# Kernel tuning notes

Hardware: AMD Instinct MI355X
Metric: run time of the kernel (lower is better)

Reference implementation:

```python
import jax, jax.numpy as jnp
import numpy as np

NEG_INF = -1e9
LEAKY_SLOPE = 0.2


def setup_inputs() -> dict:
    key = jax.random.key(0)
    k1, k2, k3, k4, k5 = jax.random.split(key, 5)
    B, N, F_in, F_out = 8, 2048, 256, 256
    x = jax.random.normal(k1, (B, N, F_in), dtype=jnp.float32)
    adj = jax.random.randint(k2, (B, N, N), 0, 2, dtype=jnp.int32)
    W = jax.random.normal(k3, (F_out, F_in), dtype=jnp.float32) * 0.05
    a_src = jax.random.normal(k4, (F_out,), dtype=jnp.float32) * 0.05
    a_dst = jax.random.normal(k5, (F_out,), dtype=jnp.float32) * 0.05
    return {"x": x, "adj": adj, "W": W, "a_src": a_src, "a_dst": a_dst}


def reference(x, adj, W, a_src, a_dst):
    # h: (B, N, F_out)
    h = jnp.einsum("bnf,of->bno", x, W)
    # a([h_i ; h_j]) == h_i @ a_src + h_j @ a_dst  (avoids O(N^2, 2F) concat)
    s_src = h @ a_src  # (B, N) score contribution of row node i
    s_dst = h @ a_dst  # (B, N) score contribution of col node j
    e = s_src[:, :, None] + s_dst[:, None, :]  # (B, N, N)
    e = jax.nn.leaky_relu(e, negative_slope=LEAKY_SLOPE)
    e = jnp.where(adj == 0, jnp.float32(NEG_INF), e)
    alpha = jax.nn.softmax(e, axis=-1)  # dropout is identity in eval mode
    h_prime = jnp.einsum("bij,bjo->bio", alpha, h)
    return h_prime
```

## Files before the change

kernel.cpp:

```cpp
#include <hip/hip_runtime.h>
#include <hip/hip_bf16.h>
#include <cstdint>
#include <cstddef>

typedef __attribute__((ext_vector_type(8))) short short8;
typedef __attribute__((ext_vector_type(4))) short short4v;
typedef __attribute__((ext_vector_type(4))) float floatx4;
typedef __attribute__((ext_vector_type(16))) float floatx16;
typedef unsigned short ushort_t;

#define LOG2E 1.44269504088896340736f

__device__ __forceinline__ unsigned short f2bf(float f) {
    unsigned u = __float_as_uint(f);
    u += 0x7FFFu + ((u >> 16) & 1u);
    return (unsigned short)(u >> 16);
}
__device__ __forceinline__ float bf2f(unsigned short s) {
    return __uint_as_float(((unsigned)s) << 16);
}

__global__ __launch_bounds__(1024) void gemm_h(const float* __restrict__ x,
                                               const float* __restrict__ W,
                                               ushort_t* __restrict__ hT,
                                               const float* __restrict__ a_src,
                                               const float* __restrict__ a_dst,
                                               float* __restrict__ s_src,
                                               float* __restrict__ s_dst) {
    const int tid = threadIdx.x;
    const int w = tid >> 6, lane = tid & 63;
    const int q = lane >> 4, t16 = lane & 15;
    const int jg = w >> 2, og = w & 3;

    __shared__ ushort_t wt[256][72];
    __shared__ float sred[2][4][64];

    const int jrow = blockIdx.x * 64 + jg * 16 + t16;
    const float* xr = x + (size_t)jrow * 256 + q * 8;
    short8 af[8];
#pragma unroll
    for (int kb = 0; kb < 8; ++kb) {
        float4 v0 = *(const float4*)(xr + kb * 32);
        float4 v1 = *(const float4*)(xr + kb * 32 + 4);
        short8 a;
        a[0] = (short)f2bf(v0.x); a[1] = (short)f2bf(v0.y);
        a[2] = (short)f2bf(v0.z); a[3] = (short)f2bf(v0.w);
        a[4] = (short)f2bf(v1.x); a[5] = (short)f2bf(v1.y);
        a[6] = (short)f2bf(v1.z); a[7] = (short)f2bf(v1.w);
        af[kb] = a;
    }

    floatx4 acc[4] = {};
#pragma unroll
    for (int kp = 0; kp < 4; ++kp) {
        if (kp) __syncthreads();
#pragma unroll
        for (int r = 0; r < 2; ++r) {
            int G = tid + 1024 * r;
            int row = G >> 3, g = G & 7;
            const float* wsrc = W + (size_t)row * 256 + kp * 64 + g * 8;
            float4 f0 = *(const float4*)(wsrc);
            float4 f1 = *(const float4*)(wsrc + 4);
            short8 wv;
            wv[0] = (short)f2bf(f0.x); wv[1] = (short)f2bf(f0.y);
            wv[2] = (short)f2bf(f0.z); wv[3] = (short)f2bf(f0.w);
            wv[4] = (short)f2bf(f1.x); wv[5] = (short)f2bf(f1.y);
            wv[6] = (short)f2bf(f1.z); wv[7] = (short)f2bf(f1.w);
            *(short8*)(&wt[row][g * 8]) = wv;
        }
        __syncthreads();
#pragma unroll
        for (int ks = 0; ks < 2; ++ks) {
#pragma unroll
            for (int ct = 0; ct < 4; ++ct) {
                short8 bf = *(const short8*)(&wt[og * 64 + ct * 16 + t16][ks * 32 + q * 8]);
                acc[ct] = __builtin_amdgcn_mfma_f32_16x16x32_bf16(af[kp * 2 + ks], bf, acc[ct], 0, 0, 0);
            }
        }
    }

    const int jbase = blockIdx.x * 64 + jg * 16 + q * 4;
    const int b = jbase >> 11, jj = jbase & 2047;
#pragma unroll
    for (int ct = 0; ct < 4; ++ct) {
        const int o = og * 64 + ct * 16 + t16;
        short4v sv;
        sv[0] = (short)f2bf(acc[ct][0]);
        sv[1] = (short)f2bf(acc[ct][1]);
        sv[2] = (short)f2bf(acc[ct][2]);
        sv[3] = (short)f2bf(acc[ct][3]);
        *(short4v*)(hT + ((size_t)b * 256 + o) * 2048 + jj) = sv;
    }

    float psv[4] = {}, pdv[4] = {};
#pragma unroll
    for (int ct = 0; ct < 4; ++ct) {
        const int o = og * 64 + ct * 16 + t16;
        float as = a_src[o], ad = a_dst[o];
#pragma unroll
        for (int r = 0; r < 4; ++r) {
            psv[r] = __fmaf_rn(acc[ct][r], as, psv[r]);
            pdv[r] = __fmaf_rn(acc[ct][r], ad, pdv[r]);
        }
    }
#pragma unroll
    for (int m = 1; m < 16; m <<= 1) {
#pragma unroll
        for (int r = 0; r < 4; ++r) {
            psv[r] += __shfl_xor(psv[r], m);
            pdv[r] += __shfl_xor(pdv[r], m);
        }
    }
    if (t16 == 0) {
#pragma unroll
        for (int r = 0; r < 4; ++r) {
            sred[0][og][jg * 16 + q * 4 + r] = psv[r];
            sred[1][og][jg * 16 + q * 4 + r] = pdv[r];
        }
    }
    __syncthreads();
    if (tid < 64) {
        float ss = sred[0][0][tid] + sred[0][1][tid] + sred[0][2][tid] + sred[0][3][tid];
        float dd = sred[1][0][tid] + sred[1][1][tid] + sred[1][2][tid] + sred[1][3][tid];
        s_src[blockIdx.x * 64 + tid] = ss;
        s_dst[blockIdx.x * 64 + tid] = dd;
    }
}

__global__ __launch_bounds__(1024) void attn(const ushort_t* __restrict__ hT,
                                             const int* __restrict__ adj,
                                             const float* __restrict__ s_src,
                                             const float* __restrict__ s_dst,
                                             float* __restrict__ out) {
    const int tid = threadIdx.x;
    const int w = tid >> 6;
    const int lane = tid & 63;
    const int l5 = lane & 31, hi = lane >> 5;
    const int b = blockIdx.x;
    const int i0 = blockIdx.y * 64;

    __shared__ ushort_t ps[2][64][72];
    __shared__ float sdl[2048];
    __shared__ float rls[64];

    const float* sdb = s_dst + (size_t)b * 2048;
    {
        int idx = tid * 2;
        float2 v = *(const float2*)(sdb + idx);
        v.x *= LOG2E; v.y *= LOG2E;
        *(float2*)(&sdl[idx]) = v;
    }

    const int ip = tid >> 4, jq = tid & 15;
    const float si = s_src[(size_t)b * 2048 + i0 + ip] * LOG2E;
    const int* adjr = adj + ((size_t)b * 2048 + i0 + ip) * 2048 + jq * 4;

    const int osub = (w & 7) * 32, ih = (w >> 3) * 32;
    const ushort_t* hTg = hT + ((size_t)b * 256 + osub + l5) * 2048 + hi * 8;

    floatx16 acc = {};
    float lsum = 0.f;
    int4 aE, aO;
    short8 af0[4], af1[4];

    aE = *(const int4*)(adjr);
    aO = *(const int4*)(adjr + 64);
#pragma unroll
    for (int ks = 0; ks < 4; ++ks)
        af0[ks] = *(const short8*)(hTg + ks * 16);
    __syncthreads();

#pragma unroll 1
    for (int it = 0; it < 16; ++it) {
        const int sc = it * 2;
        {
            float4 sd = *(const float4*)(&sdl[sc * 64 + jq * 4]);
            float sv[4] = {sd.x, sd.y, sd.z, sd.w};
            int mv[4] = {aE.x, aE.y, aE.z, aE.w};
            short4v pv;
#pragma unroll
            for (int e = 0; e < 4; ++e) {
                float t = si + sv[e];
                float lr = fmaxf(t, 0.2f * t);
                float pe = __builtin_amdgcn_exp2f(lr);
                pe = (mv[e] != 0) ? pe : 0.0f;
                unsigned short u = f2bf(pe);
                lsum += bf2f(u);
                pv[e] = (short)u;
            }
            *(short4v*)(&ps[0][ip][jq * 4]) = pv;
        }
        {
            const int nc = (sc + 2 < 32) ? sc + 2 : 31;
            aE = *(const int4*)(adjr + (size_t)nc * 64);
        }
#pragma unroll
        for (int ks = 0; ks < 4; ++ks)
            af1[ks] = *(const short8*)(hTg + (size_t)(sc + 1) * 64 + ks * 16);
        __syncthreads();
#pragma unroll
        for (int ks = 0; ks < 4; ++ks) {
            short8 bfr = *(const short8*)(&ps[0][ih + l5][ks * 16 + hi * 8]);
            acc = __builtin_amdgcn_mfma_f32_32x32x16_bf16(af0[ks], bfr, acc, 0, 0, 0);
        }
        {
            float4 sd = *(const float4*)(&sdl[(sc + 1) * 64 + jq * 4]);
            float sv[4] = {sd.x, sd.y, sd.z, sd.w};
            int mv[4] = {aO.x, aO.y, aO.z, aO.w};
            short4v pv;
#pragma unroll
            for (int e = 0; e < 4; ++e) {
                float t = si + sv[e];
                float lr = fmaxf(t, 0.2f * t);
                float pe = __builtin_amdgcn_exp2f(lr);
                pe = (mv[e] != 0) ? pe : 0.0f;
                unsigned short u = f2bf(pe);
                lsum += bf2f(u);
                pv[e] = (short)u;
            }
            *(short4v*)(&ps[1][ip][jq * 4]) = pv;
        }
        {
            const int nc = (sc + 3 < 32) ? sc + 3 : 31;
            aO = *(const int4*)(adjr + (size_t)nc * 64);
        }
        {
            const int na = (sc + 2 < 32) ? sc + 2 : 31;
#pragma unroll
            for (int ks = 0; ks < 4; ++ks)
                af0[ks] = *(const short8*)(hTg + (size_t)na * 64 + ks * 16);
        }
        __syncthreads();
#pragma unroll
        for (int ks = 0; ks < 4; ++ks) {
            short8 bfr = *(const short8*)(&ps[1][ih + l5][ks * 16 + hi * 8]);
            acc = __builtin_amdgcn_mfma_f32_32x32x16_bf16(af1[ks], bfr, acc, 0, 0, 0);
        }
    }

#pragma unroll
    for (int m = 1; m < 16; m <<= 1) lsum += __shfl_xor(lsum, m);
    if (jq == 0) rls[ip] = lsum;
    __syncthreads();

    {
        const int i = ih + l5;
        const float s = rls[i];
        const float rl = (s > 0.f) ? 1.0f / s : 0.0f;
        float* orow = out + ((size_t)b * 2048 + i0 + i) * 256 + osub;
#pragma unroll
        for (int rq = 0; rq < 4; ++rq) {
            floatx4 v;
            v[0] = acc[rq * 4 + 0] * rl;
            v[1] = acc[rq * 4 + 1] * rl;
            v[2] = acc[rq * 4 + 2] * rl;
            v[3] = acc[rq * 4 + 3] * rl;
            *(floatx4*)(orow + rq * 8 + hi * 4) = v;
        }
    }
}

extern "C" void kernel_launch(void* const* d_in, const int* in_sizes, int n_in,
                              void* d_out, int out_size, void* d_ws, size_t ws_size,
                              hipStream_t stream) {
    const float* x     = (const float*)d_in[0];
    const int*   adj   = (const int*)d_in[1];
    const float* W     = (const float*)d_in[2];
    const float* a_src = (const float*)d_in[3];
    const float* a_dst = (const float*)d_in[4];
    float* out = (float*)d_out;

    char* ws = (char*)d_ws;
    ushort_t* hT = (ushort_t*)ws;
    float* s_src = (float*)(ws + (size_t)8 * 1024 * 1024);
    float* s_dst = s_src + 16384;

    gemm_h<<<256, 1024, 0, stream>>>(x, W, hT, a_src, a_dst, s_src, s_dst);
    attn<<<dim3(8, 32), 1024, 0, stream>>>(hT, adj, s_src, s_dst, out);
}
```

Before: 273.2 us.

## Split attention into smaller blocks over rows and feature halves with LDS-staged h

The attention kernel now uses 256-thread blocks covering 32 query rows and half of the output features, launching four times as many blocks. The h tiles are staged through double-buffered shared memory instead of per-wave register loads, with a 32-column j chunk. This aims to raise occupancy and CU utilisation. In exchange, adjacency reads and exp computation are duplicated across the two feature halves.

```diff
diff --git a/kernel.cpp b/kernel.cpp
--- a/kernel.cpp
+++ b/kernel.cpp
@@ -127,54 +127,62 @@
     }
 }
 
-__global__ __launch_bounds__(1024) void attn(const ushort_t* __restrict__ hT,
-                                             const int* __restrict__ adj,
-                                             const float* __restrict__ s_src,
-                                             const float* __restrict__ s_dst,
-                                             float* __restrict__ out) {
+__global__ __launch_bounds__(256) void attn(const ushort_t* __restrict__ hT,
+                                            const int* __restrict__ adj,
+                                            const float* __restrict__ s_src,
+                                            const float* __restrict__ s_dst,
+                                            float* __restrict__ out) {
     const int tid = threadIdx.x;
     const int w = tid >> 6;
     const int lane = tid & 63;
     const int l5 = lane & 31, hi = lane >> 5;
     const int b = blockIdx.x;
-    const int i0 = blockIdx.y * 64;
-
-    __shared__ ushort_t ps[2][64][72];
+    const int i0 = blockIdx.y * 32;
+    const int ob = blockIdx.z * 128;
+
+    __shared__ ushort_t hts[2][128][40];
+    __shared__ ushort_t ps[2][32][40];
     __shared__ float sdl[2048];
-    __shared__ float rls[64];
+    __shared__ float rls[32];
 
     const float* sdb = s_dst + (size_t)b * 2048;
     {
-        int idx = tid * 2;
-        float2 v = *(const float2*)(sdb + idx);
-        v.x *= LOG2E; v.y *= LOG2E;
-        *(float2*)(&sdl[idx]) = v;
-    }
-
-    const int ip = tid >> 4, jq = tid & 15;
+        float4 v0 = *(const float4*)(sdb + tid * 8);
+        float4 v1 = *(const float4*)(sdb + tid * 8 + 4);
+        v0.x *= LOG2E; v0.y *= LOG2E; v0.z *= LOG2E; v0.w *= LOG2E;
+        v1.x *= LOG2E; v1.y *= LOG2E; v1.z *= LOG2E; v1.w *= LOG2E;
+        *(float4*)(&sdl[tid * 8]) = v0;
+        *(float4*)(&sdl[tid * 8 + 4]) = v1;
+    }
+
+    const int ip = tid >> 3, jq = tid & 7;
     const float si = s_src[(size_t)b * 2048 + i0 + ip] * LOG2E;
     const int* adjr = adj + ((size_t)b * 2048 + i0 + ip) * 2048 + jq * 4;
 
-    const int osub = (w & 7) * 32, ih = (w >> 3) * 32;
-    const ushort_t* hTg = hT + ((size_t)b * 256 + osub + l5) * 2048 + hi * 8;
+    const int srow = tid >> 2, sseg = tid & 3;
+    const ushort_t* hTg0 = hT + ((size_t)b * 256 + ob + srow) * 2048 + sseg * 8;
+    const ushort_t* hTg1 = hTg0 + (size_t)64 * 2048;
+
+    const int osub = w * 32;
 
     floatx16 acc = {};
     float lsum = 0.f;
     int4 aE, aO;
-    short8 af0[4], af1[4];
+    int4 hA0, hA1;
 
     aE = *(const int4*)(adjr);
-    aO = *(const int4*)(adjr + 64);
-#pragma unroll
-    for (int ks = 0; ks < 4; ++ks)
-        af0[ks] = *(const short8*)(hTg + ks * 16);
+    aO = *(const int4*)(adjr + 32);
+    hA0 = *(const int4*)(hTg0);
+    hA1 = *(const int4*)(hTg1);
     __syncthreads();
 
 #pragma unroll 1
-    for (int it = 0; it < 16; ++it) {
-        const int sc = it * 2;
+    for (int it = 0; it < 32; ++it) {
+        const int c = it * 2;
+        *(int4*)(&hts[0][srow][sseg * 8]) = hA0;
+        *(int4*)(&hts[0][srow + 64][sseg * 8]) = hA1;
         {
-            float4 sd = *(const float4*)(&sdl[sc * 64 + jq * 4]);
+            float4 sd = *(const float4*)(&sdl[c * 32 + jq * 4]);
             float sv[4] = {sd.x, sd.y, sd.z, sd.w};
             int mv[4] = {aE.x, aE.y, aE.z, aE.w};
             short4v pv;
@@ -190,21 +198,20 @@
             }
             *(short4v*)(&ps[0][ip][jq * 4]) = pv;
         }
+        hA0 = *(const int4*)(hTg0 + (size_t)(c + 1) * 32);
+        hA1 = *(const int4*)(hTg1 + (size_t)(c + 1) * 32);
+        aE = *(const int4*)(adjr + (size_t)((c + 2 < 64) ? c + 2 : 63) * 32);
+        __syncthreads();
+#pragma unroll
+        for (int ks = 0; ks < 2; ++ks) {
+            short8 afr = *(const short8*)(&hts[0][osub + l5][ks * 16 + hi * 8]);
+            short8 bfr = *(const short8*)(&ps[0][l5][ks * 16 + hi * 8]);
+            acc = __builtin_amdgcn_mfma_f32_32x32x16_bf16(afr, bfr, acc, 0, 0, 0);
+        }
+        *(int4*)(&hts[1][srow][sseg * 8]) = hA0;
+        *(int4*)(&hts[1][srow + 64][sseg * 8]) = hA1;
         {
-            const int nc = (sc + 2 < 32) ? sc + 2 : 31;
-            aE = *(const int4*)(adjr + (size_t)nc * 64);
-        }
-#pragma unroll
-        for (int ks = 0; ks < 4; ++ks)
-            af1[ks] = *(const short8*)(hTg + (size_t)(sc + 1) * 64 + ks * 16);
-        __syncthreads();
-#pragma unroll
-        for (int ks = 0; ks < 4; ++ks) {
-            short8 bfr = *(const short8*)(&ps[0][ih + l5][ks * 16 + hi * 8]);
-            acc = __builtin_amdgcn_mfma_f32_32x32x16_bf16(af0[ks], bfr, acc, 0, 0, 0);
-        }
-        {
-            float4 sd = *(const float4*)(&sdl[(sc + 1) * 64 + jq * 4]);
+            float4 sd = *(const float4*)(&sdl[(c + 1) * 32 + jq * 4]);
             float sv[4] = {sd.x, sd.y, sd.z, sd.w};
             int mv[4] = {aO.x, aO.y, aO.z, aO.w};
             short4v pv;
@@ -221,33 +228,30 @@
             *(short4v*)(&ps[1][ip][jq * 4]) = pv;
         }
         {
-            const int nc = (sc + 3 < 32) ? sc + 3 : 31;
-            aO = *(const int4*)(adjr + (size_t)nc * 64);
-        }
-        {
-            const int na = (sc + 2 < 32) ? sc + 2 : 31;
-#pragma unroll
-            for (int ks = 0; ks < 4; ++ks)
-                af0[ks] = *(const short8*)(hTg + (size_t)na * 64 + ks * 16);
-        }
+            const int nh = (c + 2 < 64) ? c + 2 : 63;
+            hA0 = *(const int4*)(hTg0 + (size_t)nh * 32);
+            hA1 = *(const int4*)(hTg1 + (size_t)nh * 32);
+        }
+        aO = *(const int4*)(adjr + (size_t)((c + 3 < 64) ? c + 3 : 63) * 32);
         __syncthreads();
 #pragma unroll
-        for (int ks = 0; ks < 4; ++ks) {
-            short8 bfr = *(const short8*)(&ps[1][ih + l5][ks * 16 + hi * 8]);
-            acc = __builtin_amdgcn_mfma_f32_32x32x16_bf16(af1[ks], bfr, acc, 0, 0, 0);
-        }
-    }
-
-#pragma unroll
-    for (int m = 1; m < 16; m <<= 1) lsum += __shfl_xor(lsum, m);
+        for (int ks = 0; ks < 2; ++ks) {
+            short8 afr = *(const short8*)(&hts[1][osub + l5][ks * 16 + hi * 8]);
+            short8 bfr = *(const short8*)(&ps[1][l5][ks * 16 + hi * 8]);
+            acc = __builtin_amdgcn_mfma_f32_32x32x16_bf16(afr, bfr, acc, 0, 0, 0);
+        }
+    }
+
+#pragma unroll
+    for (int m = 1; m < 8; m <<= 1) lsum += __shfl_xor(lsum, m);
     if (jq == 0) rls[ip] = lsum;
     __syncthreads();
 
     {
-        const int i = ih + l5;
+        const int i = l5;
         const float s = rls[i];
         const float rl = (s > 0.f) ? 1.0f / s : 0.0f;
-        float* orow = out + ((size_t)b * 2048 + i0 + i) * 256 + osub;
+        float* orow = out + ((size_t)b * 2048 + i0 + i) * 256 + ob + osub;
 #pragma unroll
         for (int rq = 0; rq < 4; ++rq) {
             floatx4 v;
@@ -276,5 +280,5 @@
     float* s_dst = s_src + 16384;
 
     gemm_h<<<256, 1024, 0, stream>>>(x, W, hT, a_src, a_dst, s_src, s_dst);
-    attn<<<dim3(8, 32), 1024, 0, stream>>>(hT, adj, s_src, s_dst, out);
-}
+    attn<<<dim3(8, 64, 2), 256, 0, stream>>>(hT, adj, s_src, s_dst, out);
+}
```

New measurement: 271.3 us. About the same (-0.7%).
